# Optimization experiments

Measured on AMD Instinct MI355X. Metric: run time of the kernel, lower is better.

The kernel has to match this reference:

```python
import jax, jax.numpy as jnp
import numpy as np

BATCH = 8192
EMBED_DIM = 256
INPUT_DIM = 3 * EMBED_DIM  # 768
NUM_LAYERS = 4
VOCAB_SIZES = [100000, 100000, 1000]
EPS = 1e-5


def setup_inputs() -> dict:
    key = jax.random.key(0)
    ks = jax.random.split(key, 20)
    inp = {}
    inp["x_p"] = jax.random.randint(ks[0], (BATCH,), 0, VOCAB_SIZES[0])
    inp["x_a"] = jax.random.randint(ks[1], (BATCH,), 0, VOCAB_SIZES[1])
    inp["x_c"] = jax.random.randint(ks[2], (BATCH,), 0, VOCAB_SIZES[2])
    inp["y_true"] = jax.random.uniform(ks[3], (BATCH, 1), dtype=jnp.float32)
    # embedding tables (nn.Embedding default init N(0,1))
    inp["E0"] = jax.random.normal(ks[4], (VOCAB_SIZES[0], EMBED_DIM), dtype=jnp.float32)
    inp["E1"] = jax.random.normal(ks[5], (VOCAB_SIZES[1], EMBED_DIM), dtype=jnp.float32)
    inp["E2"] = jax.random.normal(ks[6], (VOCAB_SIZES[2], EMBED_DIM), dtype=jnp.float32)
    lim = 1.0 / np.sqrt(INPUT_DIM)
    inp["Wd"] = jax.random.uniform(ks[7], (NUM_LAYERS, INPUT_DIM, INPUT_DIM), jnp.float32, -lim, lim)
    inp["bd"] = jnp.zeros((NUM_LAYERS, INPUT_DIM), jnp.float32)
    inp["Ws"] = jax.random.uniform(ks[8], (NUM_LAYERS, INPUT_DIM, INPUT_DIM), jnp.float32, -lim, lim)
    inp["bs"] = jnp.zeros((NUM_LAYERS, INPUT_DIM), jnp.float32)
    inp["wfd"] = jax.random.uniform(ks[9], (INPUT_DIM,), jnp.float32, -lim, lim)
    inp["bfd"] = jax.random.uniform(ks[10], (), jnp.float32, -lim, lim)
    inp["wfs"] = jax.random.uniform(ks[11], (INPUT_DIM,), jnp.float32, -lim, lim)
    inp["bfs"] = jax.random.uniform(ks[12], (), jnp.float32, -lim, lim)
    return inp


def _cross_network(x, W, b, net_id, mask_key):
    # per layer: cross = x @ W[l].T + b[l]; mask = bernoulli(sigmoid(layernorm over FULL tensor)); x += cross*mask
    for l in range(NUM_LAYERS):
        cross = jnp.einsum("bd,od->bo", x, W[l]) + b[l]
        m = jnp.mean(cross)
        v = jnp.mean(jnp.square(cross - m))  # F.layer_norm(x, x.size()): normalize over all elements
        ln = (cross - m) * jax.lax.rsqrt(v + EPS)
        p = jax.nn.sigmoid(ln)
        k = jax.random.fold_in(mask_key, net_id * NUM_LAYERS + l)
        mask = jax.random.bernoulli(k, p).astype(x.dtype)
        x = x + cross * mask
    return x


def _bce(p, y):
    return jnp.mean(-(y * jnp.log(p) + (1.0 - y) * jnp.log(1.0 - p)))


def reference(x_p, x_a, x_c, y_true, E0, E1, E2, Wd, bd, Ws, bs, wfd, bfd, wfs, bfs):
    h = EMBED_DIM // 2
    e0, e1, e2 = E0[x_p], E1[x_a], E2[x_c]  # [B, embed_dim] each
    e_a = jnp.concatenate([e0[:, :h], e1[:, :h], e2[:, :h]], axis=-1)
    e_b = jnp.concatenate([e0[:, h:], e1[:, h:], e2[:, h:]], axis=-1)
    x = jnp.concatenate([e_a, e_b], axis=-1)  # [B, 3*embed_dim]

    mask_key = jax.random.key(42)
    x_d = _cross_network(x, Wd, bd, 0, mask_key)
    x_s = _cross_network(x, Ws, bs, 1, mask_key)

    sd_d = jax.nn.sigmoid(x_d @ wfd + bfd)[:, None]  # fc_d(x_d)
    ss_s = jax.nn.sigmoid(x_s @ wfs + bfs)[:, None]  # fc_s(x_s)
    sd_s = jax.nn.sigmoid(x_s @ wfd + bfd)[:, None]  # fc_d(x_s)
    ss_d = jax.nn.sigmoid(x_d @ wfs + bfs)[:, None]  # fc_s(x_d)
    y_pred_d = 0.5 * (sd_d + ss_s)
    y_pred_s = 0.5 * (sd_s + ss_d)

    loss_d = _bce(y_pred_d, y_true)
    loss_s = _bce(y_pred_s, y_true)
    bce_loss = loss_d + loss_s
    weight_d = jnp.maximum(0.0, loss_d - bce_loss)
    weight_s = jnp.maximum(0.0, loss_s - bce_loss)
    tri_loss = bce_loss + weight_d * loss_d + weight_s * loss_s
    return (y_pred_d, tri_loss)
```

## Files before the change

### kernel.cpp

```cpp
#include <hip/hip_runtime.h>
#include <hip/hip_bf16.h>
#include <cstdint>
#include <cstddef>

#define BATCH   8192
#define DIM     768
#define NTOT    6291456
#define NLAYERS 4

typedef _Float16 half8 __attribute__((ext_vector_type(8)));
typedef float    f32x4 __attribute__((ext_vector_type(4)));

#define AS_GLOBAL __attribute__((address_space(1)))
#define AS_LDS    __attribute__((address_space(3)))

__device__ __forceinline__ void async_copy16(const void* g, void* l) {
  __builtin_amdgcn_global_load_lds((AS_GLOBAL const uint32_t*)g,
                                   (AS_LDS uint32_t*)l, 16, 0, 0);
}


__host__ __device__ __forceinline__ uint32_t rotl32(uint32_t v, int d) {
  return (v << d) | (v >> (32 - d));
}

__host__ __device__ __forceinline__ void threefry2x32(
    uint32_t k0, uint32_t k1, uint32_t x0, uint32_t x1,
    uint32_t& o0, uint32_t& o1) {
  uint32_t ks2 = k0 ^ k1 ^ 0x1BD11BDAu;
  x0 += k0; x1 += k1;
#define TF_R(r) { x0 += x1; x1 = rotl32(x1, (r)) ^ x0; }
  TF_R(13) TF_R(15) TF_R(26) TF_R(6)
  x0 += k1; x1 += ks2 + 1u;
  TF_R(17) TF_R(29) TF_R(16) TF_R(24)
  x0 += ks2; x1 += k0 + 2u;
  TF_R(13) TF_R(15) TF_R(26) TF_R(6)
  x0 += k0; x1 += k1 + 3u;
  TF_R(17) TF_R(29) TF_R(16) TF_R(24)
  x0 += k1; x1 += ks2 + 4u;
  TF_R(13) TF_R(15) TF_R(26) TF_R(6)
  x0 += ks2; x1 += k0 + 5u;
#undef TF_R
  o0 = x0; o1 = x1;
}

__device__ __forceinline__ double sigmoid_d(double x) {
  return 1.0 / (1.0 + exp(-x));
}

__device__ __forceinline__ double dexp(double x) {
  x = fmin(fmax(x, -708.0), 708.0);
  const double LOG2E = 1.4426950408889634;
  const double LN2   = 0.6931471805599453;
  double t = x * LOG2E;
  double n = rint(t);
  double g = (t - n) * LN2;
  double r = 2.7557319223985893e-07;
  r = r * g + 2.7557319223985888e-06;
  r = r * g + 2.4801587301587302e-05;
  r = r * g + 1.9841269841269841e-04;
  r = r * g + 1.3888888888888889e-03;
  r = r * g + 8.3333333333333332e-03;
  r = r * g + 4.1666666666666664e-02;
  r = r * g + 1.6666666666666666e-01;
  r = r * g + 0.5;
  r = r * g + 1.0;
  r = r * g + 1.0;
  int ni = (int)n;
  double sc = __longlong_as_double(((long long)(1023 + ni)) << 52);
  return r * sc;
}

__global__ __launch_bounds__(256) void gather_kernel(
    const int* __restrict__ x_p, const int* __restrict__ x_a,
    const int* __restrict__ x_c,
    const float* __restrict__ E0, const float* __restrict__ E1,
    const float* __restrict__ E2,
    _Float16* __restrict__ xdh, _Float16* __restrict__ xdl,
    _Float16* __restrict__ xsh, _Float16* __restrict__ xsl,
    double* __restrict__ stats, double* __restrict__ bce_acc) {
  if (blockIdx.x == 0 && threadIdx.x < 18) {
    if (threadIdx.x < 16) stats[threadIdx.x] = 0.0;
    else bce_acc[threadIdx.x - 16] = 0.0;
  }
  int gid = blockIdx.x * 256 + threadIdx.x;
  int g = gid >> 13;
  int b = gid & 8191;
  int f0 = g * 8;
  int half_ = f0 >= 384;
  int w = f0 - 384 * half_;
  int tbl = w >> 7;
  int c0 = (w & 127) + (half_ << 7);
  int row;
  const float* E;
  if (tbl == 0)      { E = E0; row = x_p[b]; }
  else if (tbl == 1) { E = E1; row = x_a[b]; }
  else               { E = E2; row = x_c[b]; }
  const float* src = &E[(size_t)row * 256 + c0];
  f32x4 v0 = *(const f32x4*)src;
  f32x4 v1 = *(const f32x4*)(src + 4);
  half8 h, l;
#pragma unroll
  for (int i = 0; i < 4; ++i) {
    h[i] = (_Float16)v0[i];
    l[i] = (_Float16)(v0[i] - (float)h[i]);
    h[i + 4] = (_Float16)v1[i];
    l[i + 4] = (_Float16)(v1[i] - (float)h[i + 4]);
  }
  size_t o = (size_t)gid * 8;
  *(half8*)&xdh[o] = h; *(half8*)&xdl[o] = l;
  *(half8*)&xsh[o] = h; *(half8*)&xsl[o] = l;
}

__global__ __launch_bounds__(256) void split_w_kernel(
    const float* __restrict__ Wd, const float* __restrict__ Ws,
    _Float16* __restrict__ Wh, _Float16* __restrict__ Wl) {
  int gid = blockIdx.x * 256 + threadIdx.x;
  int nl = gid / 73728;
  int r3 = gid - nl * 73728;
  int t  = r3 / 3072;
  int r4 = r3 - t * 3072;
  int kk = r4 / 768;
  int row = r4 - kk * 768;
  int k0 = t * 32 + kk * 8;
  const float* src = ((nl < 4) ? Wd : Ws) +
                     ((size_t)(nl & 3) * 768 + row) * 768 + k0;
  f32x4 v0 = *(const f32x4*)src;
  f32x4 v1 = *(const f32x4*)(src + 4);
  half8 h, l;
#pragma unroll
  for (int i = 0; i < 4; ++i) {
    h[i] = (_Float16)v0[i];
    l[i] = (_Float16)(v0[i] - (float)h[i]);
    h[i + 4] = (_Float16)v1[i];
    l[i + 4] = (_Float16)(v1[i] - (float)h[i + 4]);
  }
  size_t o = (size_t)gid * 8;
  *(half8*)&Wh[o] = h;
  *(half8*)&Wl[o] = l;
}

__global__ __launch_bounds__(512, 4) void gemm_mfma_kernel(
    const _Float16* __restrict__ xdh, const _Float16* __restrict__ xdl,
    const _Float16* __restrict__ xsh, const _Float16* __restrict__ xsl,
    const _Float16* __restrict__ Wh, const _Float16* __restrict__ Wl,
    const float* __restrict__ bd, const float* __restrict__ bs,
    float* __restrict__ crd, float* __restrict__ crs,
    double* __restrict__ stats, int layer) {
  const int net = blockIdx.z;
  const float* bias = (net ? bs : bd) + layer * DIM;
  float* C = net ? crs : crd;

  const int tid  = threadIdx.x;
  const int wave = tid >> 6, lane = tid & 63;
  const int quad = lane >> 4, l16 = lane & 15;
  const int m0 = blockIdx.x * 128;
  const int n0 = blockIdx.y * 192;

  __shared__ _Float16 lds[2 * 16384];

  const _Float16* xh = net ? xsh : xdh;
  const _Float16* xl = net ? xsl : xdl;
  const size_t wpanel = ((size_t)net * NLAYERS + layer) * (size_t)(24 * 4 * 768 * 8);
  const _Float16* wh = Wh + wpanel;
  const _Float16* wl = Wl + wpanel;

  const _Float16* gp[4];
  int gstr[4];
  int dbyte[4];
#pragma unroll
  for (int j = 0; j < 4; ++j) {
    int sb = wave * 256 + j * 64;
    dbyte[j] = sb * 16;
    int s = sb + lane;
    if (s < 512) {
      int kk = s >> 7, r = s & 127;
      gp[j] = xh + (size_t)(kk * 8192 + m0 + r) * 8;
      gstr[j] = 4 * 8192 * 8;
    } else {
      int s2 = s - 512;
      int s3 = (s2 >= 768) ? s2 - 768 : s2;
      int kk = (s3 * 683) >> 17;
      int r  = s3 - kk * 192;
      gp[j] = ((s2 >= 768) ? wl : wh) + (size_t)(kk * 768 + n0 + r) * 8;
      gstr[j] = 4 * 768 * 8;
    }
  }

  const int wm = (wave >> 2) * 64;
  const int wn = (wave & 3) * 48;

  const _Float16* alb = xl + (size_t)(quad * 8192 + m0 + wm + l16) * 8;

  f32x4 acc[4][3];
#pragma unroll
  for (int i = 0; i < 4; ++i)
#pragma unroll
    for (int j = 0; j < 3; ++j) acc[i][j] = (f32x4){0.f, 0.f, 0.f, 0.f};

#pragma unroll
  for (int j = 0; j < 4; ++j)
    async_copy16(gp[j], (char*)lds + dbyte[j]);
  __syncthreads();

  int cur = 0;
  for (int t = 0; t < 24; ++t) {
    if (t < 23) {
#pragma unroll
      for (int j = 0; j < 4; ++j)
        async_copy16(gp[j] + (t + 1) * gstr[j],
                     (char*)lds + (cur ^ 1) * 32768 + dbyte[j]);
    }
    const _Float16* alt = alb + t * 262144;
    half8 al[4];
#pragma unroll
    for (int mt = 0; mt < 4; ++mt)
      al[mt] = *(const half8*)(alt + mt * 128);

    const _Float16* L = lds + cur * 16384;
    half8 ah[4], bh[3], bl[3];
#pragma unroll
    for (int mt = 0; mt < 4; ++mt)
      ah[mt] = *(const half8*)&L[(quad * 128 + wm + mt * 16 + l16) * 8];
#pragma unroll
    for (int nt = 0; nt < 3; ++nt) {
      int ss = 512 + quad * 192 + wn + nt * 16 + l16;
      bh[nt] = *(const half8*)&L[ss * 8];
      bl[nt] = *(const half8*)&L[ss * 8 + 6144];
    }
    __builtin_amdgcn_s_setprio(1);
#pragma unroll
    for (int nt = 0; nt < 3; ++nt)
#pragma unroll
      for (int mt = 0; mt < 4; ++mt)
        acc[mt][nt] = __builtin_amdgcn_mfma_f32_16x16x32_f16(ah[mt], bh[nt], acc[mt][nt], 0, 0, 0);
#pragma unroll
    for (int nt = 0; nt < 3; ++nt)
#pragma unroll
      for (int mt = 0; mt < 4; ++mt)
        acc[mt][nt] = __builtin_amdgcn_mfma_f32_16x16x32_f16(ah[mt], bl[nt], acc[mt][nt], 0, 0, 0);
#pragma unroll
    for (int nt = 0; nt < 3; ++nt)
#pragma unroll
      for (int mt = 0; mt < 4; ++mt)
        acc[mt][nt] = __builtin_amdgcn_mfma_f32_16x16x32_f16(al[mt], bh[nt], acc[mt][nt], 0, 0, 0);
    __builtin_amdgcn_s_setprio(0);
    __syncthreads();
    cur ^= 1;
  }

  float biasv[3];
#pragma unroll
  for (int nt = 0; nt < 3; ++nt) biasv[nt] = bias[n0 + wn + nt * 16 + l16];

  double S = 0.0, Q = 0.0;
#pragma unroll
  for (int mt = 0; mt < 4; ++mt) {
#pragma unroll
    for (int nt = 0; nt < 3; ++nt) {
      int n = n0 + wn + nt * 16 + l16;
      size_t gbase = (size_t)(n >> 4) * 131072;
#pragma unroll
      for (int r = 0; r < 4; ++r) {
        int m = m0 + wm + mt * 16 + quad * 4 + r;
        float v = acc[mt][nt][r] + biasv[nt];
        C[gbase + m * 16 + l16] = v;
        S += (double)v;
        Q += (double)v * (double)v;
      }
    }
  }
#pragma unroll
  for (int off = 32; off > 0; off >>= 1) {
    S += __shfl_down(S, off);
    Q += __shfl_down(Q, off);
  }
  double* red = (double*)lds;
  if (lane == 0) { red[wave * 2] = S; red[wave * 2 + 1] = Q; }
  __syncthreads();
  if (tid == 0) {
    double s2 = 0.0, q2 = 0.0;
#pragma unroll
    for (int wv = 0; wv < 8; ++wv) { s2 += red[wv * 2]; q2 += red[wv * 2 + 1]; }
    double* st = stats + ((size_t)layer * 2 + net) * 2;
    atomicAdd(&st[0], s2);
    atomicAdd(&st[1], q2);
  }
}

__global__ __launch_bounds__(256) void mask_update_kernel(
    _Float16* __restrict__ xdh, _Float16* __restrict__ xdl,
    _Float16* __restrict__ xsh, _Float16* __restrict__ xsl,
    const float* __restrict__ crd, const float* __restrict__ crs,
    const double* __restrict__ stats, int layer,
    uint32_t kd0, uint32_t kd1, uint32_t ks0, uint32_t ks1) {
  const int net = blockIdx.y;
  _Float16* xh = net ? xsh : xdh;
  _Float16* xl = net ? xsl : xdl;
  const float* cr = net ? crs : crd;
  const uint32_t k0 = net ? ks0 : kd0;
  const uint32_t k1 = net ? ks1 : kd1;

  const double invN = 1.0 / (double)NTOT;
  const double* st = stats + ((size_t)layer * 2 + net) * 2;
  double meand = st[0] * invN;
  double vard  = st[1] * invN - meand * meand;
  float m  = (float)meand;
  float sv = (float)vard + 1e-5f;
  float rs = (float)(1.0 / sqrt((double)sv));

  int cg = blockIdx.x * 256 + threadIdx.x;
  int g16 = cg >> 13;
  int b   = cg & 8191;
  int f0  = g16 * 16;

  f32x4 c4[4];
#pragma unroll
  for (int i = 0; i < 4; ++i) c4[i] = *(const f32x4*)&cr[(size_t)cg * 16 + i * 4];

  size_t xg0 = ((size_t)g16 * 2) * 8192 + b;
  half8 h0 = *(const half8*)&xh[xg0 * 8];
  half8 l0 = *(const half8*)&xl[xg0 * 8];
  half8 h1 = *(const half8*)&xh[(xg0 + 8192) * 8];
  half8 l1 = *(const half8*)&xl[(xg0 + 8192) * 8];
  half8 ho0, lo0, ho1, lo1;

#pragma unroll
  for (int i = 0; i < 16; ++i) {
    float c  = c4[i >> 2][i & 3];
    float ln = (c - m) * rs;
    uint32_t o0, o1;
    threefry2x32(k0, k1, 0u, (uint32_t)(b * 768 + f0 + i), o0, o1);
    uint32_t bits = o0 ^ o1;
    float u = __uint_as_float(0x3F800000u | (bits >> 9)) - 1.0f;
    double e  = dexp(-(double)ln);
    double ue = (double)u;
    float xv = (i < 8) ? ((float)h0[i & 7] + (float)l0[i & 7])
                       : ((float)h1[i & 7] + (float)l1[i & 7]);
    if (ue + ue * e < 1.0) xv += c;
    _Float16 hh = (_Float16)xv;
    _Float16 ll = (_Float16)(xv - (float)hh);
    if (i < 8) { ho0[i & 7] = hh; lo0[i & 7] = ll; }
    else       { ho1[i & 7] = hh; lo1[i & 7] = ll; }
  }
  *(half8*)&xh[xg0 * 8] = ho0;
  *(half8*)&xl[xg0 * 8] = lo0;
  *(half8*)&xh[(xg0 + 8192) * 8] = ho1;
  *(half8*)&xl[(xg0 + 8192) * 8] = lo1;
}

__global__ __launch_bounds__(256) void head_kernel(
    const _Float16* __restrict__ xdh, const _Float16* __restrict__ xdl,
    const _Float16* __restrict__ xsh, const _Float16* __restrict__ xsl,
    const float* __restrict__ wfd, const float* __restrict__ wfs,
    const float* __restrict__ bfd_p, const float* __restrict__ bfs_p,
    const float* __restrict__ y_true,
    float* __restrict__ out, double* __restrict__ bce_acc) {
  const int tq = threadIdx.x >> 6;
  const int tb = threadIdx.x & 63;
  const int row = blockIdx.x * 64 + tb;

  float dd = 0.f, dsw = 0.f, sd = 0.f, ssw = 0.f;
  const int g0 = tq * 24;
  for (int g = g0; g < g0 + 24; ++g) {
    size_t o = ((size_t)g * 8192 + row) * 8;
    half8 hd = *(const half8*)&xdh[o];
    half8 ld = *(const half8*)&xdl[o];
    half8 hs = *(const half8*)&xsh[o];
    half8 ls = *(const half8*)&xsl[o];
#pragma unroll
    for (int i = 0; i < 8; ++i) {
      float vd = (float)hd[i] + (float)ld[i];
      float vs = (float)hs[i] + (float)ls[i];
      float wd = wfd[g * 8 + i], ws = wfs[g * 8 + i];
      dd  = fmaf(vd, wd, dd);
      dsw = fmaf(vd, ws, dsw);
      sd  = fmaf(vs, wd, sd);
      ssw = fmaf(vs, ws, ssw);
    }
  }
  __shared__ float part[4][64][4];
  part[tq][tb][0] = dd;  part[tq][tb][1] = dsw;
  part[tq][tb][2] = sd;  part[tq][tb][3] = ssw;
  __syncthreads();

  if (threadIdx.x < 64) {
    float DD  = part[0][tb][0] + part[1][tb][0] + part[2][tb][0] + part[3][tb][0];
    float DSW = part[0][tb][1] + part[1][tb][1] + part[2][tb][1] + part[3][tb][1];
    float SD  = part[0][tb][2] + part[1][tb][2] + part[2][tb][2] + part[3][tb][2];
    float SSW = part[0][tb][3] + part[1][tb][3] + part[2][tb][3] + part[3][tb][3];
    float bfd = *bfd_p, bfs = *bfs_p;
    double sdd = sigmoid_d((double)(DD + bfd));
    double ssd = sigmoid_d((double)(DSW + bfs));
    double sds = sigmoid_d((double)(SD + bfd));
    double sss = sigmoid_d((double)(SSW + bfs));
    double ypd = 0.5 * (sdd + sss);
    double yps = 0.5 * (sds + ssd);
    out[row] = (float)ypd;
    double y = (double)y_true[row];
    double bce_d = -(y * log(ypd) + (1.0 - y) * log(1.0 - ypd));
    double bce_s = -(y * log(yps) + (1.0 - y) * log(1.0 - yps));
#pragma unroll
    for (int off = 32; off > 0; off >>= 1) {
      bce_d += __shfl_down(bce_d, off);
      bce_s += __shfl_down(bce_s, off);
    }
    if (tb == 0) {
      atomicAdd(&bce_acc[0], bce_d);
      atomicAdd(&bce_acc[1], bce_s);
    }
  }
}

__global__ void loss_kernel(const double* __restrict__ bce_acc,
                            float* __restrict__ out_tri) {
  if (threadIdx.x == 0) {
    double loss_d = bce_acc[0] / (double)BATCH;
    double loss_s = bce_acc[1] / (double)BATCH;
    double bce = loss_d + loss_s;
    double wd = fmax(0.0, loss_d - bce);
    double ws = fmax(0.0, loss_s - bce);
    out_tri[0] = (float)(bce + wd * loss_d + ws * loss_s);
  }
}

extern "C" void kernel_launch(void* const* d_in, const int* in_sizes, int n_in,
                              void* d_out, int out_size, void* d_ws, size_t ws_size,
                              hipStream_t stream) {
  const int* x_p = (const int*)d_in[0];
  const int* x_a = (const int*)d_in[1];
  const int* x_c = (const int*)d_in[2];
  const float* y_true = (const float*)d_in[3];
  const float* E0 = (const float*)d_in[4];
  const float* E1 = (const float*)d_in[5];
  const float* E2 = (const float*)d_in[6];
  const float* Wd = (const float*)d_in[7];
  const float* bd = (const float*)d_in[8];
  const float* Ws = (const float*)d_in[9];
  const float* bs = (const float*)d_in[10];
  const float* wfd = (const float*)d_in[11];
  const float* bfd = (const float*)d_in[12];
  const float* wfs = (const float*)d_in[13];
  const float* bfs = (const float*)d_in[14];
  float* out = (float*)d_out;

  char* p = (char*)d_ws;
  float* crd = (float*)p;                 p += (size_t)NTOT * 4;
  float* crs = (float*)p;                 p += (size_t)NTOT * 4;
  double* stats   = (double*)p;           p += (size_t)16 * 8;
  double* bce_acc = (double*)p;           p += (size_t)2 * 8;
  _Float16* xdh = (_Float16*)p;           p += (size_t)NTOT * 2;
  _Float16* xdl = (_Float16*)p;           p += (size_t)NTOT * 2;
  _Float16* xsh = (_Float16*)p;           p += (size_t)NTOT * 2;
  _Float16* xsl = (_Float16*)p;           p += (size_t)NTOT * 2;
  _Float16* Wh  = (_Float16*)p;           p += (size_t)2 * NLAYERS * DIM * DIM * 2;
  _Float16* Wl  = (_Float16*)p;           p += (size_t)2 * NLAYERS * DIM * DIM * 2;

  gather_kernel<<<NTOT / 8 / 256, 256, 0, stream>>>(
      x_p, x_a, x_c, E0, E1, E2, xdh, xdl, xsh, xsl, stats, bce_acc);
  split_w_kernel<<<2 * NLAYERS * DIM * DIM / 8 / 256, 256, 0, stream>>>(
      Wd, Ws, Wh, Wl);

  for (int l = 0; l < NLAYERS; ++l) {
    gemm_mfma_kernel<<<dim3(64, 4, 2), 512, 0, stream>>>(
        xdh, xdl, xsh, xsl, Wh, Wl, bd, bs, crd, crs, stats, l);
    uint32_t kd0, kd1, ks0, ks1;
    threefry2x32(0u, 42u, 0u, (uint32_t)l, kd0, kd1);
    threefry2x32(0u, 42u, 0u, (uint32_t)(4 + l), ks0, ks1);
    mask_update_kernel<<<dim3(NTOT / 16 / 256, 2), 256, 0, stream>>>(
        xdh, xdl, xsh, xsl, crd, crs, stats, l, kd0, kd1, ks0, ks1);
  }

  head_kernel<<<BATCH / 64, 256, 0, stream>>>(
      xdh, xdl, xsh, xsl, wfd, wfs, bfd, bfs, y_true, out, bce_acc);
  loss_kernel<<<1, 64, 0, stream>>>(bce_acc, out + BATCH);
}
```

Before: 667.9 us.

## Enlarge GEMM tile to 256x192 and stage x-low via LDS with phased MFMA

Doubles the GEMM block tile in M (256 rows), which halves the grid to 32x4x2 blocks, and gives each wave a 64x96 sub-tile. The low half of x is now loaded into LDS with async copies instead of direct global reads. The prefetch wait uses explicit vmcnt waits and raw barriers, and the work is split into three phases of LDS reads plus MFMAs. The aim is more data reuse per LDS byte and better overlap of loads with math. The cost is higher register and LDS use (lower occupancy, launch_bounds now 2) and only 256 blocks, which may underfill the 256 CUs.

```diff
diff --git a/kernel.cpp b/kernel.cpp
--- a/kernel.cpp
+++ b/kernel.cpp
@@ -140,7 +140,7 @@
   *(half8*)&Wl[o] = l;
 }
 
-__global__ __launch_bounds__(512, 4) void gemm_mfma_kernel(
+__global__ __launch_bounds__(512, 2) void gemm_mfma_kernel(
     const _Float16* __restrict__ xdh, const _Float16* __restrict__ xdl,
     const _Float16* __restrict__ xsh, const _Float16* __restrict__ xsl,
     const _Float16* __restrict__ Wh, const _Float16* __restrict__ Wl,
@@ -154,10 +154,10 @@
   const int tid  = threadIdx.x;
   const int wave = tid >> 6, lane = tid & 63;
   const int quad = lane >> 4, l16 = lane & 15;
-  const int m0 = blockIdx.x * 128;
+  const int m0 = blockIdx.x * 256;
   const int n0 = blockIdx.y * 192;
 
-  __shared__ _Float16 lds[2 * 16384];
+  __shared__ _Float16 lds[2 * 28672];
 
   const _Float16* xh = net ? xsh : xdh;
   const _Float16* xl = net ? xsl : xdl;
@@ -165,20 +165,21 @@
   const _Float16* wh = Wh + wpanel;
   const _Float16* wl = Wl + wpanel;
 
-  const _Float16* gp[4];
-  int gstr[4];
-  int dbyte[4];
-#pragma unroll
-  for (int j = 0; j < 4; ++j) {
-    int sb = wave * 256 + j * 64;
+  const _Float16* gp[7];
+  int gstr[7];
+  int dbyte[7];
+#pragma unroll
+  for (int j = 0; j < 7; ++j) {
+    int sb = wave * 448 + j * 64;
     dbyte[j] = sb * 16;
     int s = sb + lane;
-    if (s < 512) {
-      int kk = s >> 7, r = s & 127;
-      gp[j] = xh + (size_t)(kk * 8192 + m0 + r) * 8;
+    if (s < 2048) {
+      int s2 = s & 1023;
+      int kk = s2 >> 8, r = s2 & 255;
+      gp[j] = ((s < 1024) ? xh : xl) + (size_t)(kk * 8192 + m0 + r) * 8;
       gstr[j] = 4 * 8192 * 8;
     } else {
-      int s2 = s - 512;
+      int s2 = s - 2048;
       int s3 = (s2 >= 768) ? s2 - 768 : s2;
       int kk = (s3 * 683) >> 17;
       int r  = s3 - kk * 192;
@@ -187,77 +188,118 @@
     }
   }
 
-  const int wm = (wave >> 2) * 64;
-  const int wn = (wave & 3) * 48;
-
-  const _Float16* alb = xl + (size_t)(quad * 8192 + m0 + wm + l16) * 8;
-
-  f32x4 acc[4][3];
+  const int wm = (wave >> 1) * 64;
+  const int wn = (wave & 1) * 96;
+
+  f32x4 acc[4][6];
 #pragma unroll
   for (int i = 0; i < 4; ++i)
 #pragma unroll
-    for (int j = 0; j < 3; ++j) acc[i][j] = (f32x4){0.f, 0.f, 0.f, 0.f};
-
-#pragma unroll
-  for (int j = 0; j < 4; ++j)
+    for (int j = 0; j < 6; ++j) acc[i][j] = (f32x4){0.f, 0.f, 0.f, 0.f};
+
+#pragma unroll
+  for (int j = 0; j < 7; ++j)
     async_copy16(gp[j], (char*)lds + dbyte[j]);
-  __syncthreads();
 
   int cur = 0;
   for (int t = 0; t < 24; ++t) {
+    __builtin_amdgcn_s_barrier();
     if (t < 23) {
 #pragma unroll
-      for (int j = 0; j < 4; ++j)
+      for (int j = 0; j < 7; ++j)
         async_copy16(gp[j] + (t + 1) * gstr[j],
-                     (char*)lds + (cur ^ 1) * 32768 + dbyte[j]);
-    }
-    const _Float16* alt = alb + t * 262144;
-    half8 al[4];
-#pragma unroll
-    for (int mt = 0; mt < 4; ++mt)
-      al[mt] = *(const half8*)(alt + mt * 128);
-
-    const _Float16* L = lds + cur * 16384;
-    half8 ah[4], bh[3], bl[3];
-#pragma unroll
-    for (int mt = 0; mt < 4; ++mt)
-      ah[mt] = *(const half8*)&L[(quad * 128 + wm + mt * 16 + l16) * 8];
-#pragma unroll
-    for (int nt = 0; nt < 3; ++nt) {
-      int ss = 512 + quad * 192 + wn + nt * 16 + l16;
+                     (char*)lds + (cur ^ 1) * 57344 + dbyte[j]);
+      asm volatile("s_waitcnt vmcnt(7)" ::: "memory");
+    } else {
+      asm volatile("s_waitcnt vmcnt(0)" ::: "memory");
+    }
+    __builtin_amdgcn_sched_barrier(0);
+    __builtin_amdgcn_s_barrier();
+
+    const _Float16* L = lds + cur * 28672;
+    half8 ah[4], al[4], bh[2], bl[2];
+
+#pragma unroll
+    for (int mt = 0; mt < 4; ++mt) {
+      int sl = quad * 256 + wm + mt * 16 + l16;
+      ah[mt] = *(const half8*)&L[sl * 8];
+      al[mt] = *(const half8*)&L[sl * 8 + 8192];
+    }
+#pragma unroll
+    for (int nt = 0; nt < 2; ++nt) {
+      int ss = 2048 + quad * 192 + wn + nt * 16 + l16;
       bh[nt] = *(const half8*)&L[ss * 8];
       bl[nt] = *(const half8*)&L[ss * 8 + 6144];
     }
+    __builtin_amdgcn_s_barrier();
     __builtin_amdgcn_s_setprio(1);
 #pragma unroll
-    for (int nt = 0; nt < 3; ++nt)
-#pragma unroll
-      for (int mt = 0; mt < 4; ++mt)
-        acc[mt][nt] = __builtin_amdgcn_mfma_f32_16x16x32_f16(ah[mt], bh[nt], acc[mt][nt], 0, 0, 0);
-#pragma unroll
-    for (int nt = 0; nt < 3; ++nt)
-#pragma unroll
-      for (int mt = 0; mt < 4; ++mt)
-        acc[mt][nt] = __builtin_amdgcn_mfma_f32_16x16x32_f16(ah[mt], bl[nt], acc[mt][nt], 0, 0, 0);
-#pragma unroll
-    for (int nt = 0; nt < 3; ++nt)
-#pragma unroll
-      for (int mt = 0; mt < 4; ++mt)
-        acc[mt][nt] = __builtin_amdgcn_mfma_f32_16x16x32_f16(al[mt], bh[nt], acc[mt][nt], 0, 0, 0);
+    for (int nt = 0; nt < 2; ++nt)
+#pragma unroll
+      for (int mt = 0; mt < 4; ++mt) {
+        f32x4 a = acc[mt][nt];
+        a = __builtin_amdgcn_mfma_f32_16x16x32_f16(ah[mt], bh[nt], a, 0, 0, 0);
+        a = __builtin_amdgcn_mfma_f32_16x16x32_f16(al[mt], bh[nt], a, 0, 0, 0);
+        a = __builtin_amdgcn_mfma_f32_16x16x32_f16(ah[mt], bl[nt], a, 0, 0, 0);
+        acc[mt][nt] = a;
+      }
     __builtin_amdgcn_s_setprio(0);
-    __syncthreads();
+    __builtin_amdgcn_s_barrier();
+
+#pragma unroll
+    for (int nt = 0; nt < 2; ++nt) {
+      int ss = 2048 + quad * 192 + wn + (nt + 2) * 16 + l16;
+      bh[nt] = *(const half8*)&L[ss * 8];
+      bl[nt] = *(const half8*)&L[ss * 8 + 6144];
+    }
+    __builtin_amdgcn_s_barrier();
+    __builtin_amdgcn_s_setprio(1);
+#pragma unroll
+    for (int nt = 0; nt < 2; ++nt)
+#pragma unroll
+      for (int mt = 0; mt < 4; ++mt) {
+        f32x4 a = acc[mt][nt + 2];
+        a = __builtin_amdgcn_mfma_f32_16x16x32_f16(ah[mt], bh[nt], a, 0, 0, 0);
+        a = __builtin_amdgcn_mfma_f32_16x16x32_f16(al[mt], bh[nt], a, 0, 0, 0);
+        a = __builtin_amdgcn_mfma_f32_16x16x32_f16(ah[mt], bl[nt], a, 0, 0, 0);
+        acc[mt][nt + 2] = a;
+      }
+    __builtin_amdgcn_s_setprio(0);
+    __builtin_amdgcn_s_barrier();
+
+#pragma unroll
+    for (int nt = 0; nt < 2; ++nt) {
+      int ss = 2048 + quad * 192 + wn + (nt + 4) * 16 + l16;
+      bh[nt] = *(const half8*)&L[ss * 8];
+      bl[nt] = *(const half8*)&L[ss * 8 + 6144];
+    }
+    __builtin_amdgcn_s_barrier();
+    __builtin_amdgcn_s_setprio(1);
+#pragma unroll
+    for (int nt = 0; nt < 2; ++nt)
+#pragma unroll
+      for (int mt = 0; mt < 4; ++mt) {
+        f32x4 a = acc[mt][nt + 4];
+        a = __builtin_amdgcn_mfma_f32_16x16x32_f16(ah[mt], bh[nt], a, 0, 0, 0);
+        a = __builtin_amdgcn_mfma_f32_16x16x32_f16(al[mt], bh[nt], a, 0, 0, 0);
+        a = __builtin_amdgcn_mfma_f32_16x16x32_f16(ah[mt], bl[nt], a, 0, 0, 0);
+        acc[mt][nt + 4] = a;
+      }
+    __builtin_amdgcn_s_setprio(0);
     cur ^= 1;
   }
 
-  float biasv[3];
-#pragma unroll
-  for (int nt = 0; nt < 3; ++nt) biasv[nt] = bias[n0 + wn + nt * 16 + l16];
+  __syncthreads();
+
+  float biasv[6];
+#pragma unroll
+  for (int nt = 0; nt < 6; ++nt) biasv[nt] = bias[n0 + wn + nt * 16 + l16];
 
   double S = 0.0, Q = 0.0;
 #pragma unroll
   for (int mt = 0; mt < 4; ++mt) {
 #pragma unroll
-    for (int nt = 0; nt < 3; ++nt) {
+    for (int nt = 0; nt < 6; ++nt) {
       int n = n0 + wn + nt * 16 + l16;
       size_t gbase = (size_t)(n >> 4) * 131072;
 #pragma unroll
@@ -462,7 +504,7 @@
       Wd, Ws, Wh, Wl);
 
   for (int l = 0; l < NLAYERS; ++l) {
-    gemm_mfma_kernel<<<dim3(64, 4, 2), 512, 0, stream>>>(
+    gemm_mfma_kernel<<<dim3(32, 4, 2), 512, 0, stream>>>(
         xdh, xdl, xsh, xsl, Wh, Wl, bd, bs, crd, crs, stats, l);
     uint32_t kd0, kd1, ks0, ks1;
     threefry2x32(0u, 42u, 0u, (uint32_t)l, kd0, kd1);
```

After: 643.5 us. 1.04x faster.
